# Kernel optimization log

Measured on AMD Instinct MI355X. Metric: run time of the kernel, lower is better.

## Reference

```python
import jax, jax.numpy as jnp
import numpy as np

BIT = 8      # shared-exponent mantissa bits (bf_conf.*_bit)
GSZ = 36     # block size (bf_conf.*_sz)


def bfp_quantize(x, bit=BIT, sz=GSZ):
    """Block floating point: groups of `sz` consecutive elements share one
    exponent e = floor(log2(max|x|)); each element keeps `bit` mantissa bits."""
    shape = x.shape
    flat = x.reshape(-1)
    n = flat.shape[0]
    pad = (-n) % sz
    flat = jnp.pad(flat, (0, pad))
    g = flat.reshape(-1, sz)                                   # [G, sz]
    maxabs = jnp.max(jnp.abs(g), axis=1, keepdims=True)
    e = jnp.floor(jnp.log2(jnp.where(maxabs > 0, maxabs, 1.0)))
    scale = jnp.exp2(e - (bit - 1))                            # lsb of shared-exp format
    q = jnp.round(g / scale) * scale
    q = jnp.where(maxabs > 0, q, 0.0)
    return q.reshape(-1)[:n].reshape(shape)


def setup_inputs() -> dict:
    key = jax.random.key(0)
    k1, k2, k3 = jax.random.split(key, 3)
    B, Cin, Cout, H, W, K = 16, 32, 32, 224, 224, 3
    x = jax.random.normal(k1, (B, Cin, H, W), dtype=jnp.float32)
    fan_in = Cin * K * K
    bound = 1.0 / np.sqrt(fan_in)
    weight = jax.random.uniform(k2, (Cout, Cin, K, K), jnp.float32, -bound, bound)
    bias = jax.random.uniform(k3, (Cout,), jnp.float32, -bound, bound)
    return {"x": x, "weight": weight, "bias": bias}


def reference(x, weight, bias):
    xq = bfp_quantize(x)          # f_i
    wq = bfp_quantize(weight)     # f_w
    out = jax.lax.conv_general_dilated(
        xq, wq,
        window_strides=(1, 1),
        padding=((1, 1), (1, 1)),
        rhs_dilation=(1, 1),
        feature_group_count=1,
        dimension_numbers=("NCHW", "OIHW", "NCHW"),
    )
    out = out + bias[None, :, None, None]
    out = bfp_quantize(out)       # f_o
    return out
```

## Files before the change

kernel.cpp:

```cpp
#include <hip/hip_runtime.h>
#include <hip/hip_bf16.h>

#define GSZ 36
static const int NX  = 16 * 32 * 224 * 224;
static const int NX4 = NX / 4;
static const int NW  = 32 * 32 * 3 * 3;
static const int GXN = (NX + GSZ - 1) / GSZ;
static const int HWp = 224 * 224;

typedef short bf16x8 __attribute__((ext_vector_type(8)));
typedef float f32x4  __attribute__((ext_vector_type(4)));

__device__ __forceinline__ unsigned div36(unsigned n) {
    return (unsigned)(((unsigned long long)n * 954437177ull) >> 35);
}
__device__ __forceinline__ float scale_from_max(float m) {
    int e = (int)((__float_as_uint(m) >> 23) & 0xffu) - 127;
    return __uint_as_float((unsigned)(e + 120) << 23);
}
__device__ __forceinline__ float inv_from_scale(float s) {
    return __uint_as_float(0x7F000000u - __float_as_uint(s));
}
__device__ __forceinline__ unsigned short f2bf(float f) {
    return (unsigned short)(__float_as_uint(f) >> 16);
}

__global__ void k_quant_wt(const float* __restrict__ w, unsigned short* __restrict__ wt) {
    int g = threadIdx.x;
    int base = g * GSZ;
    float v[GSZ];
    const float4* p = reinterpret_cast<const float4*>(w + base);
    #pragma unroll
    for (int i = 0; i < 9; ++i) {
        float4 t = p[i];
        v[4*i+0] = t.x; v[4*i+1] = t.y; v[4*i+2] = t.z; v[4*i+3] = t.w;
    }
    float m = 0.0f;
    #pragma unroll
    for (int i = 0; i < GSZ; ++i) m = fmaxf(m, fabsf(v[i]));
    if (m > 0.0f) {
        float s = scale_from_max(m), inv = inv_from_scale(s);
        #pragma unroll
        for (int i = 0; i < GSZ; ++i) v[i] = rintf(v[i] * inv) * s;
    }
    #pragma unroll
    for (int i = 0; i < GSZ; ++i) {
        int f = base + i;
        int co = f / 288, rem = f - co * 288;
        int ci = rem / 9, s = rem - ci * 9;
        wt[s * 1024 + co * 32 + ci] = f2bf(v[i]);
    }
}

#define TSTR 452
__global__ __launch_bounds__(256, 4) void k_quant_x_fused(const float* __restrict__ x,
                                                          unsigned short* __restrict__ xt) {
    __shared__ unsigned short tile[32 * TSTR];

    int t = threadIdx.x;
    int b = blockIdx.y, hp = blockIdx.x;
    int F0 = (b * 32) * HWp + hp * 448;

    #pragma unroll
    for (int it = 0; it < 2; ++it) {
        int task = t + 256 * it;
        if (task < 448) {
            int ci = (task * 2341) >> 15;
            int gi = task - ci * 14;
            int F = F0 + ci * HWp;
            int r = F - 36 * (int)div36((unsigned)F);
            int rel0 = 36 * gi - r;
            if (rel0 < 448) {
                int g4 = (int)(((unsigned)(F - r)) >> 2) + 9 * gi;
                f32x4 v[9];
                #pragma unroll
                for (int i = 0; i < 9; ++i) {
                    f32x4 tv = {0.f, 0.f, 0.f, 0.f};
                    int f4 = g4 + i;
                    if ((unsigned)f4 < (unsigned)NX4)
                        tv = reinterpret_cast<const f32x4*>(x)[f4];
                    v[i] = tv;
                }
                float m = 0.f;
                #pragma unroll
                for (int i = 0; i < 9; ++i)
                    #pragma unroll
                    for (int k = 0; k < 4; ++k) m = fmaxf(m, fabsf(v[i][k]));
                if (m > 0.f) {
                    float s = scale_from_max(m), inv = inv_from_scale(s);
                    #pragma unroll
                    for (int i = 0; i < 9; ++i)
                        #pragma unroll
                        for (int k = 0; k < 4; ++k)
                            v[i][k] = rintf(v[i][k] * inv) * s;
                }
                #pragma unroll
                for (int i = 0; i < 9; ++i) {
                    int rel = rel0 + 4 * i;
                    if ((unsigned)rel < 448u) {
                        uint2 o;
                        o.x = (unsigned)f2bf(v[i][0]) | ((unsigned)f2bf(v[i][1]) << 16);
                        o.y = (unsigned)f2bf(v[i][2]) | ((unsigned)f2bf(v[i][3]) << 16);
                        *reinterpret_cast<uint2*>(&tile[ci * TSTR + rel]) = o;
                    }
                }
            }
        }
    }
    __syncthreads();

    unsigned short* ob = xt + ((size_t)b * HWp + hp * 448) * 32;
    for (int j = 0; j < 7; ++j) {
        int qd = t + 256 * j;
        int px = qd >> 2;
        int c0 = (qd & 3) * 8;
        unsigned uu[4];
        #pragma unroll
        for (int p = 0; p < 4; ++p) {
            unsigned short lo = tile[(c0 + 2 * p) * TSTR + px];
            unsigned short hi = tile[(c0 + 2 * p + 1) * TSTR + px];
            uu[p] = (unsigned)lo | ((unsigned)hi << 16);
        }
        *reinterpret_cast<uint4*>(ob + (size_t)px * 32 + c0) =
            make_uint4(uu[0], uu[1], uu[2], uu[3]);
    }
}

#define PXS 40
__global__ __launch_bounds__(256, 2) void k_conv_mfma(const unsigned short* __restrict__ xt,
                                                      const unsigned short* __restrict__ wt,
                                                      const float* __restrict__ bias,
                                                      float* __restrict__ out) {
    __shared__ __align__(16) unsigned short xs[18 * 34 * PXS];

    int tid  = threadIdx.x;
    int lane = tid & 63;
    int wid  = tid >> 6;
    int b  = blockIdx.z;
    int h0 = blockIdx.y * 16;
    int w0 = blockIdx.x * 32;

    const unsigned short* xb = xt + (size_t)b * HWp * 32;
    #pragma unroll
    for (int k = 0; k < 10; ++k) {
        int q = tid + k * 256;
        if (q < 2448) {
            int r = q / 136;
            int rem = q - r * 136;
            int p = rem >> 2, ch = rem & 3;
            int gh = h0 + r - 1, gw = w0 + p - 1;
            uint4 val = make_uint4(0u, 0u, 0u, 0u);
            if ((unsigned)gh < 224u && (unsigned)gw < 224u)
                val = *reinterpret_cast<const uint4*>(xb + ((size_t)(gh * 224 + gw)) * 32 + ch * 8);
            *reinterpret_cast<uint4*>(&xs[(r * 34 + p) * PXS + ch * 8]) = val;
        }
    }

    bf16x8 Wf[9][2];
    #pragma unroll
    for (int s = 0; s < 9; ++s)
        #pragma unroll
        for (int hf = 0; hf < 2; ++hf)
            Wf[s][hf] = *reinterpret_cast<const bf16x8*>(
                wt + s * 1024 + (hf * 16 + (lane & 15)) * 32 + (lane >> 4) * 8);

    int m4 = (lane >> 4) << 2;
    f32x4 acc[8][2];
    {
        f32x4 b0, b1;
        #pragma unroll
        for (int r = 0; r < 4; ++r) {
            b0[r] = bias[m4 + r];
            b1[r] = bias[16 + m4 + r];
        }
        #pragma unroll
        for (int g = 0; g < 8; ++g) { acc[g][0] = b0; acc[g][1] = b1; }
    }

    __syncthreads();

    int row4 = wid << 2;
    int kchunk = (lane >> 4) << 3;
    #pragma unroll
    for (int s = 0; s < 9; ++s) {
        int kh = s / 3, kw = s - kh * 3;
        #pragma unroll
        for (int g = 0; g < 8; ++g) {
            int row = row4 + (g >> 1);
            int col = ((g & 1) << 4) + (lane & 15);
            bf16x8 X = *reinterpret_cast<const bf16x8*>(
                &xs[((row + kh) * 34 + col + kw) * PXS + kchunk]);
            acc[g][0] = __builtin_amdgcn_mfma_f32_16x16x32_bf16(Wf[s][0], X, acc[g][0], 0, 0, 0);
            acc[g][1] = __builtin_amdgcn_mfma_f32_16x16x32_bf16(Wf[s][1], X, acc[g][1], 0, 0, 0);
        }
    }

    int pxl = lane & 15;
    #pragma unroll
    for (int g = 0; g < 8; ++g) {
        int h = h0 + row4 + (g >> 1);
        int wl = w0 + ((g & 1) << 4) + pxl;
        size_t base = (size_t)(b * 32) * HWp + h * 224 + wl;
        #pragma unroll
        for (int hf = 0; hf < 2; ++hf)
            #pragma unroll
            for (int r = 0; r < 4; ++r)
                out[base + (size_t)((hf << 4) + m4 + r) * HWp] = acc[g][hf][r];
    }
}

__global__ __launch_bounds__(256, 4) void k_quant_out(float* __restrict__ buf) {
    __shared__ float lds[4 * 2304];
    int t = threadIdx.x, lane = t & 63, wid = t >> 6;
    int gbase = (blockIdx.x * 4 + wid) * 64;
    int f4base = gbase * 9;

    #pragma unroll
    for (int i = 0; i < 9; ++i) {
        int f4 = f4base + i * 64 + lane;
        float4 v = make_float4(0.f, 0.f, 0.f, 0.f);
        if ((unsigned)f4 < (unsigned)NX4) v = reinterpret_cast<const float4*>(buf)[f4];
        *reinterpret_cast<float4*>(&lds[wid * 2304 + (i * 64 + lane) * 4]) = v;
    }
    __syncthreads();

    if (gbase + lane < GXN) {
        float* p = &lds[wid * 2304 + lane * 36];
        f32x4 vv[9];
        #pragma unroll
        for (int i = 0; i < 9; ++i) vv[i] = *reinterpret_cast<f32x4*>(p + 4 * i);
        float m = 0.f;
        #pragma unroll
        for (int i = 0; i < 9; ++i)
            #pragma unroll
            for (int k = 0; k < 4; ++k) m = fmaxf(m, fabsf(vv[i][k]));
        if (m > 0.f) {
            float s = scale_from_max(m), inv = inv_from_scale(s);
            #pragma unroll
            for (int i = 0; i < 9; ++i) {
                #pragma unroll
                for (int k = 0; k < 4; ++k) vv[i][k] = rintf(vv[i][k] * inv) * s;
                *reinterpret_cast<f32x4*>(p + 4 * i) = vv[i];
            }
        }
    }
    __syncthreads();

    #pragma unroll
    for (int i = 0; i < 9; ++i) {
        int f4 = f4base + i * 64 + lane;
        if ((unsigned)f4 < (unsigned)NX4)
            reinterpret_cast<float4*>(buf)[f4] =
                *reinterpret_cast<float4*>(&lds[wid * 2304 + (i * 64 + lane) * 4]);
    }
}

extern "C" void kernel_launch(void* const* d_in, const int* in_sizes, int n_in,
                              void* d_out, int out_size, void* d_ws, size_t ws_size,
                              hipStream_t stream) {
    (void)in_sizes; (void)n_in; (void)out_size; (void)ws_size;
    const float* x    = (const float*)d_in[0];
    const float* w    = (const float*)d_in[1];
    const float* bias = (const float*)d_in[2];
    float* out        = (float*)d_out;

    unsigned short* xt = (unsigned short*)d_ws;
    unsigned short* wt = xt + NX;

    k_quant_wt<<<1, 256, 0, stream>>>(w, wt);
    k_quant_x_fused<<<dim3(112, 16), 256, 0, stream>>>(x, xt);
    k_conv_mfma<<<dim3(7, 14, 16), 256, 0, stream>>>(xt, wt, bias, out);
    k_quant_out<<<2788, 256, 0, stream>>>(out);
}
```

Before: 263.6 us.

## Coalesce x loads in quant kernel with shared-memory partial maxima

```diff
diff --git a/kernel.cpp b/kernel.cpp
--- a/kernel.cpp
+++ b/kernel.cpp
@@ -55,11 +55,33 @@
 #define TSTR 452
 __global__ __launch_bounds__(256, 4) void k_quant_x_fused(const float* __restrict__ x,
                                                           unsigned short* __restrict__ xt) {
-    __shared__ unsigned short tile[32 * TSTR];
+    __shared__ __align__(16) unsigned char raw[32 * TSTR * 2];
+    unsigned short* tile = reinterpret_cast<unsigned short*>(raw);
+    float* pmax = reinterpret_cast<float*>(raw);
+    __shared__ float scl[32 * 14];
 
     int t = threadIdx.x;
     int b = blockIdx.y, hp = blockIdx.x;
     int F0 = (b * 32) * HWp + hp * 448;
+
+    int c4  = t & 127;
+    int ciB = t >> 7;
+
+    f32x4 v[16];
+    #pragma unroll
+    for (int j = 0; j < 16; ++j) {
+        int ci = ciB + 2 * j;
+        int F = F0 + ci * HWp;
+        int r = F - 36 * (int)div36((unsigned)F);
+        int f4 = (int)(((unsigned)(F - r)) >> 2) + c4;
+        f32x4 tv = {0.f, 0.f, 0.f, 0.f};
+        if ((unsigned)f4 < (unsigned)NX4)
+            tv = reinterpret_cast<const f32x4*>(x)[f4];
+        v[j] = tv;
+        pmax[ci * 128 + c4] = fmaxf(fmaxf(fabsf(tv[0]), fabsf(tv[1])),
+                                    fmaxf(fabsf(tv[2]), fabsf(tv[3])));
+    }
+    __syncthreads();
 
     #pragma unroll
     for (int it = 0; it < 2; ++it) {
@@ -67,44 +89,36 @@
         if (task < 448) {
             int ci = (task * 2341) >> 15;
             int gi = task - ci * 14;
-            int F = F0 + ci * HWp;
-            int r = F - 36 * (int)div36((unsigned)F);
-            int rel0 = 36 * gi - r;
-            if (rel0 < 448) {
-                int g4 = (int)(((unsigned)(F - r)) >> 2) + 9 * gi;
-                f32x4 v[9];
+            const float* pp = &pmax[ci * 128 + 9 * gi];
+            float m = pp[0];
+            #pragma unroll
+            for (int i = 1; i < 9; ++i) m = fmaxf(m, pp[i]);
+            scl[task] = (m > 0.f) ? scale_from_max(m) : 0.f;
+        }
+    }
+    __syncthreads();
+
+    int gi4 = (c4 * 57) >> 9;
+    #pragma unroll
+    for (int j = 0; j < 16; ++j) {
+        int ci = ciB + 2 * j;
+        int F = F0 + ci * HWp;
+        int r = F - 36 * (int)div36((unsigned)F);
+        int rel = 4 * c4 - r;
+        if ((unsigned)rel < 448u) {
+            float s = scl[ci * 14 + gi4];
+            f32x4 q = v[j];
+            if (s > 0.f) {
+                float inv = inv_from_scale(s);
                 #pragma unroll
-                for (int i = 0; i < 9; ++i) {
-                    f32x4 tv = {0.f, 0.f, 0.f, 0.f};
-                    int f4 = g4 + i;
-                    if ((unsigned)f4 < (unsigned)NX4)
-                        tv = reinterpret_cast<const f32x4*>(x)[f4];
-                    v[i] = tv;
-                }
-                float m = 0.f;
-                #pragma unroll
-                for (int i = 0; i < 9; ++i)
-                    #pragma unroll
-                    for (int k = 0; k < 4; ++k) m = fmaxf(m, fabsf(v[i][k]));
-                if (m > 0.f) {
-                    float s = scale_from_max(m), inv = inv_from_scale(s);
-                    #pragma unroll
-                    for (int i = 0; i < 9; ++i)
-                        #pragma unroll
-                        for (int k = 0; k < 4; ++k)
-                            v[i][k] = rintf(v[i][k] * inv) * s;
-                }
-                #pragma unroll
-                for (int i = 0; i < 9; ++i) {
-                    int rel = rel0 + 4 * i;
-                    if ((unsigned)rel < 448u) {
-                        uint2 o;
-                        o.x = (unsigned)f2bf(v[i][0]) | ((unsigned)f2bf(v[i][1]) << 16);
-                        o.y = (unsigned)f2bf(v[i][2]) | ((unsigned)f2bf(v[i][3]) << 16);
-                        *reinterpret_cast<uint2*>(&tile[ci * TSTR + rel]) = o;
-                    }
-                }
+                for (int k = 0; k < 4; ++k) q[k] = rintf(q[k] * inv) * s;
+            } else {
+                q = f32x4{0.f, 0.f, 0.f, 0.f};
             }
+            uint2 o;
+            o.x = (unsigned)f2bf(q[0]) | ((unsigned)f2bf(q[1]) << 16);
+            o.y = (unsigned)f2bf(q[2]) | ((unsigned)f2bf(q[3]) << 16);
+            *reinterpret_cast<uint2*>(&tile[ci * TSTR + rel]) = o;
         }
     }
     __syncthreads();
```

Result: faster. 247.4 us (-6.2%).
